# Optimization experiments

Measured on AMD Instinct MI355X. Metric: run time of the kernel, lower is better.

## Reference

```python
import jax, jax.numpy as jnp
import numpy as np

N = 50000      # nodes
E = 800000     # edges (before self-loops)
IN = 256       # in_channels
HID = 128      # hidden_channels
OUT = 128      # out_channels
NEG_SLOPE = 0.2
EPS = 1e-16


def setup_inputs() -> dict:
    key = jax.random.key(0)
    ks = jax.random.split(key, 16)
    p = lambda k, shape: jax.random.normal(k, shape, jnp.float32) * 0.1
    return {
        "x": jax.random.normal(ks[0], (N, IN), jnp.float32),
        "edge_index": jax.random.randint(ks[1], (2, E), 0, N, dtype=jnp.int64),
        # semantic MLP
        "W1": p(ks[2], (IN, HID)), "b1": jnp.zeros((HID,), jnp.float32),
        "W2": p(ks[3], (HID, HID)), "b2": jnp.zeros((HID,), jnp.float32),
        # gat1: HID -> HID//2, heads=4, concat -> 2*HID
        "g1_W": p(ks[4], (HID, 4 * (HID // 2))),
        "g1_as": p(ks[5], (4, HID // 2)), "g1_ad": p(ks[6], (4, HID // 2)),
        "g1_b": jnp.zeros((4 * (HID // 2),), jnp.float32),
        # gat2: 2*HID -> OUT, heads=2, mean -> OUT
        "g2_W": p(ks[7], (2 * HID, 2 * OUT)),
        "g2_as": p(ks[8], (2, OUT)), "g2_ad": p(ks[9], (2, OUT)),
        "g2_b": jnp.zeros((OUT,), jnp.float32),
        # gat3: OUT -> OUT, heads=1, mean -> OUT
        "g3_W": p(ks[10], (OUT, OUT)),
        "g3_as": p(ks[11], (1, OUT)), "g3_ad": p(ks[12], (1, OUT)),
        "g3_b": jnp.zeros((OUT,), jnp.float32),
    }


def _gat(h_in, src, dst, W, a_src, a_dst, bias, heads, concat, n):
    # Linear projection into heads: [n, H, C]
    h = (h_in @ W).reshape(n, heads, -1)
    alpha_s = jnp.sum(h * a_src[None], axis=-1)  # [n, H]
    alpha_d = jnp.sum(h * a_dst[None], axis=-1)  # [n, H]
    e = jax.nn.leaky_relu(alpha_s[src] + alpha_d[dst], NEG_SLOPE)  # [E', H]
    # segment softmax over edges grouped by destination node
    m = jax.ops.segment_max(e, dst, num_segments=n)
    ex = jnp.exp(e - m[dst])
    denom = jax.ops.segment_sum(ex, dst, num_segments=n)
    alpha = ex / (denom[dst] + EPS)  # [E', H]
    msg = h[src] * alpha[..., None]  # [E', H, C]
    out = jax.ops.segment_sum(msg, dst, num_segments=n)  # [n, H, C]
    out = out.reshape(n, -1) if concat else out.mean(axis=1)
    return out + bias


def reference(x, edge_index, W1, b1, W2, b2,
              g1_W, g1_as, g1_ad, g1_b,
              g2_W, g2_as, g2_ad, g2_b,
              g3_W, g3_as, g3_ad, g3_b):
    n = x.shape[0]
    # PyG GATConv add_self_loops=True: append self-loop edges once
    loops = jnp.arange(n, dtype=edge_index.dtype)
    src = jnp.concatenate([edge_index[0], loops])
    dst = jnp.concatenate([edge_index[1], loops])
    # semantic MLP (inference: dropout = identity)
    h = jax.nn.relu(x @ W1 + b1)
    h = jax.nn.relu(h @ W2 + b2)
    h = jax.nn.elu(_gat(h, src, dst, g1_W, g1_as, g1_ad, g1_b, 4, True, n))
    h = jax.nn.elu(_gat(h, src, dst, g2_W, g2_as, g2_ad, g2_b, 2, False, n))
    h = _gat(h, src, dst, g3_W, g3_as, g3_ad, g3_b, 1, False, n)
    return h
```

## Files before the change

kernel.cpp:

```cpp
#include <hip/hip_runtime.h>
#include <math.h>


#define NEG_SLOPE 0.2f
#define EPS_DEN 1e-16f

typedef __attribute__((ext_vector_type(8))) short short8;
typedef __attribute__((ext_vector_type(4))) float f32x4;
typedef __attribute__((ext_vector_type(4))) unsigned short u16x4;

__device__ inline unsigned short f2b(float f) {
  unsigned u = __builtin_bit_cast(unsigned, f);
  unsigned r = (u + 0x7fffu + ((u >> 16) & 1u)) >> 16;
  return (unsigned short)r;
}
__device__ inline float b2f(unsigned short u) {
  return __builtin_bit_cast(float, (unsigned)u << 16);
}

__device__ inline void glds16(const void* g, void* l) {
  __builtin_amdgcn_global_load_lds(
      (const __attribute__((address_space(1))) void*)g,
      (__attribute__((address_space(3))) void*)l, 16, 0, 0);
}

template <int H>
__device__ inline void loadH(const float* p, float* v) {
  if constexpr (H == 4) {
    float4 t = *(const float4*)p;
    v[0] = t.x; v[1] = t.y; v[2] = t.z; v[3] = t.w;
  } else if constexpr (H == 2) {
    float2 t = *(const float2*)p;
    v[0] = t.x; v[1] = t.y;
  } else {
    v[0] = *p;
  }
}

template <int ACT, int OBF>
__global__ __launch_bounds__(256) void mfma_gemm(
    const unsigned short* __restrict__ A, const unsigned short* __restrict__ Bt,
    const float* __restrict__ bias, float* __restrict__ Cf,
    unsigned short* __restrict__ Cb, int n, int K, int M) {
  __shared__ unsigned short As[128 * 64];
  __shared__ unsigned short Bs[128 * 64];

  const int tid = threadIdx.x;
  const int w = tid >> 6, lane = tid & 63;
  const int row0 = blockIdx.x * 128, col0 = blockIdx.y * 128;
  const int lr = lane >> 3, lg = lane & 7;
  const int lm = lane & 15, kg = lane >> 4;
  const int wm = (w >> 1) * 64, wn = (w & 1) * 64;

  f32x4 acc[4][4];
#pragma unroll
  for (int i = 0; i < 4; i++)
#pragma unroll
    for (int j = 0; j < 4; j++) acc[i][j] = {0.f, 0.f, 0.f, 0.f};

  const int swz = (lg ^ lr) << 3;

  for (int k0 = 0; k0 < K; k0 += 64) {
    __syncthreads();
#pragma unroll
    for (int it = 0; it < 4; it++) {
      const int r = w * 32 + it * 8;
      glds16(A + (size_t)(row0 + r + lr) * K + k0 + swz, &As[r * 64]);
      glds16(Bt + (size_t)(col0 + r + lr) * K + k0 + swz, &Bs[r * 64]);
    }
    __syncthreads();

#pragma unroll
    for (int kh = 0; kh < 2; kh++) {
      const int sw = ((kh * 4 + kg) ^ (lm & 7)) << 3;
      short8 aF[4], bF[4];
#pragma unroll
      for (int i = 0; i < 4; i++) {
        aF[i] = *(const short8*)&As[(wm + i * 16 + lm) * 64 + sw];
        bF[i] = *(const short8*)&Bs[(wn + i * 16 + lm) * 64 + sw];
      }
#pragma unroll
      for (int i = 0; i < 4; i++)
#pragma unroll
        for (int j = 0; j < 4; j++)
          acc[i][j] = __builtin_amdgcn_mfma_f32_16x16x32_bf16(
              aF[i], bF[j], acc[i][j], 0, 0, 0);
    }
  }

  const int r4 = kg * 4;
#pragma unroll
  for (int j = 0; j < 4; j++) {
    const int col = col0 + wn + j * 16 + lm;
    const float bv = bias ? bias[col] : 0.f;
#pragma unroll
    for (int i = 0; i < 4; i++) {
#pragma unroll
      for (int r = 0; r < 4; r++) {
        const int row = row0 + wm + i * 16 + r4 + r;
        if (row < n) {
          float v = acc[i][j][r] + bv;
          if (ACT == 1) v = v > 0.f ? v : 0.f;
          if (OBF)
            Cb[(size_t)row * M + col] = f2b(v);
          else
            Cf[(size_t)row * M + col] = v;
        }
      }
    }
  }
}

__global__ __launch_bounds__(256) void mlp_fused_kernel(
    const unsigned short* __restrict__ X, const unsigned short* __restrict__ W1t,
    const float* __restrict__ b1, const unsigned short* __restrict__ W2t,
    const float* __restrict__ b2, unsigned short* __restrict__ H2, int n) {
  __shared__ unsigned short As[128 * 64];
  __shared__ unsigned short Bs[128 * 64];
  __shared__ unsigned short H1s[128 * 136];

  const int tid = threadIdx.x;
  const int w = tid >> 6, lane = tid & 63;
  const int row0 = blockIdx.x * 128;
  const int lr = lane >> 3, lg = lane & 7;
  const int lm = lane & 15, kg = lane >> 4;
  const int wm = (w >> 1) * 64, wn = (w & 1) * 64;
  const int swz = (lg ^ lr) << 3;
  const int r4 = kg * 4;

  f32x4 acc[4][4];
#pragma unroll
  for (int i = 0; i < 4; i++)
#pragma unroll
    for (int j = 0; j < 4; j++) acc[i][j] = {0.f, 0.f, 0.f, 0.f};

  for (int k0 = 0; k0 < 256; k0 += 64) {
    __syncthreads();
#pragma unroll
    for (int it = 0; it < 4; it++) {
      const int r = w * 32 + it * 8;
      glds16(X + (size_t)(row0 + r + lr) * 256 + k0 + swz, &As[r * 64]);
      glds16(W1t + (size_t)(r + lr) * 256 + k0 + swz, &Bs[r * 64]);
    }
    __syncthreads();
#pragma unroll
    for (int kh = 0; kh < 2; kh++) {
      const int sw = ((kh * 4 + kg) ^ (lm & 7)) << 3;
      short8 aF[4], bF[4];
#pragma unroll
      for (int i = 0; i < 4; i++) {
        aF[i] = *(const short8*)&As[(wm + i * 16 + lm) * 64 + sw];
        bF[i] = *(const short8*)&Bs[(wn + i * 16 + lm) * 64 + sw];
      }
#pragma unroll
      for (int i = 0; i < 4; i++)
#pragma unroll
        for (int j = 0; j < 4; j++)
          acc[i][j] = __builtin_amdgcn_mfma_f32_16x16x32_bf16(
              aF[i], bF[j], acc[i][j], 0, 0, 0);
    }
  }

#pragma unroll
  for (int j = 0; j < 4; j++) {
    const int col = wn + j * 16 + lm;
    const float bv = b1[col];
#pragma unroll
    for (int i = 0; i < 4; i++) {
#pragma unroll
      for (int r = 0; r < 4; r++) {
        const int lrow = wm + i * 16 + r4 + r;
        float v = acc[i][j][r] + bv;
        v = v > 0.f ? v : 0.f;
        H1s[lrow * 136 + col] = f2b(v);
      }
    }
  }
#pragma unroll
  for (int i = 0; i < 4; i++)
#pragma unroll
    for (int j = 0; j < 4; j++) acc[i][j] = {0.f, 0.f, 0.f, 0.f};
  __syncthreads();

  for (int k0 = 0; k0 < 128; k0 += 64) {
    __syncthreads();
#pragma unroll
    for (int it = 0; it < 4; it++) {
      const int r = w * 32 + it * 8;
      glds16(W2t + (size_t)(r + lr) * 128 + k0 + swz, &Bs[r * 64]);
    }
    __syncthreads();
#pragma unroll
    for (int kh = 0; kh < 2; kh++) {
      const int swB = ((kh * 4 + kg) ^ (lm & 7)) << 3;
      const int kofs = k0 + (kh * 4 + kg) * 8;
      short8 aF[4], bF[4];
#pragma unroll
      for (int i = 0; i < 4; i++) {
        aF[i] = *(const short8*)&H1s[(wm + i * 16 + lm) * 136 + kofs];
        bF[i] = *(const short8*)&Bs[(wn + i * 16 + lm) * 64 + swB];
      }
#pragma unroll
      for (int i = 0; i < 4; i++)
#pragma unroll
        for (int j = 0; j < 4; j++)
          acc[i][j] = __builtin_amdgcn_mfma_f32_16x16x32_bf16(
              aF[i], bF[j], acc[i][j], 0, 0, 0);
    }
  }

#pragma unroll
  for (int j = 0; j < 4; j++) {
    const int col = wn + j * 16 + lm;
    const float bv = b2[col];
#pragma unroll
    for (int i = 0; i < 4; i++) {
#pragma unroll
      for (int r = 0; r < 4; r++) {
        const int row = row0 + wm + i * 16 + r4 + r;
        if (row < n) {
          float v = acc[i][j][r] + bv;
          v = v > 0.f ? v : 0.f;
          H2[(size_t)row * 128 + col] = f2b(v);
        }
      }
    }
  }
}

struct PrepArgs {
  const float* x; unsigned short* xb; long long nx;
  const float* W[5]; unsigned short* Wt[5];
  int K[5], M[5], t0[6];
  int* deg; int N;
};

__global__ __launch_bounds__(256) void fused_prep_kernel(PrepArgs a) {
  const int tid = threadIdx.x, bid = blockIdx.x, nb = gridDim.x;
  const long long gt = (long long)bid * 256 + tid;
  const long long gsz = (long long)nb * 256;
  __shared__ float tt[32][33];

  for (long long i = gt; i < a.N; i += gsz) a.deg[i] = 0;
  for (long long i = gt * 4; i < a.nx; i += gsz * 4) {
    float4 v = *(const float4*)(a.x + i);
    u16x4 u = {f2b(v.x), f2b(v.y), f2b(v.z), f2b(v.w)};
    *(u16x4*)(a.xb + i) = u;
  }
  for (int t = bid; t < a.t0[5]; t += nb) {
    int di = 0;
    while (t >= a.t0[di + 1]) di++;
    const int local = t - a.t0[di];
    const int K = a.K[di], M = a.M[di], mtiles = M / 32;
    const int mb = (local % mtiles) * 32, kb = (local / mtiles) * 32;
    const float* W = a.W[di];
    unsigned short* Wt = a.Wt[di];
    const int tx = tid & 31, ty = tid >> 5;
    __syncthreads();
#pragma unroll
    for (int i = 0; i < 4; i++)
      tt[ty + i * 8][tx] = W[(size_t)(kb + ty + i * 8) * M + mb + tx];
    __syncthreads();
#pragma unroll
    for (int i = 0; i < 4; i++)
      Wt[(size_t)(mb + ty + i * 8) * K + kb + tx] = f2b(tt[tx][ty + i * 8]);
  }
}

__global__ void count_deg_kernel(const int* __restrict__ edst,
                                 int* __restrict__ deg, int E, int n) {
  int i = blockIdx.x * blockDim.x + threadIdx.x;
  if (i >= E + n) return;
  int d = (i < E) ? edst[i] : (i - E);
  if ((unsigned)d < (unsigned)n) atomicAdd(&deg[d], 1);
}

__global__ __launch_bounds__(256) void block_reduce_kernel(
    const int* __restrict__ deg, int* __restrict__ bsum, int n) {
  __shared__ int s[256];
  const int t = threadIdx.x, i = blockIdx.x * 256 + t;
  s[t] = (i < n) ? deg[i] : 0;
  __syncthreads();
#pragma unroll
  for (int off = 128; off; off >>= 1) {
    if (t < off) s[t] += s[t + off];
    __syncthreads();
  }
  if (t == 0) bsum[blockIdx.x] = s[0];
}

__global__ __launch_bounds__(256) void scan_bsums_kernel(int* __restrict__ bsum,
                                                         int nb) {
  __shared__ int s[256];
  const int t = threadIdx.x;
  const int v = (t < nb) ? bsum[t] : 0;
  s[t] = v;
  __syncthreads();
#pragma unroll
  for (int off = 1; off < 256; off <<= 1) {
    int a = (t >= off) ? s[t - off] : 0;
    __syncthreads();
    s[t] += a;
    __syncthreads();
  }
  if (t < nb) bsum[t] = s[t] - v;
}

__global__ __launch_bounds__(256) void scan_final_kernel(
    const int* __restrict__ deg, const int* __restrict__ bsumx,
    int* __restrict__ rowptr, int* __restrict__ cursor, int n) {
  __shared__ int s[256];
  const int t = threadIdx.x, i = blockIdx.x * 256 + t;
  const int v = (i < n) ? deg[i] : 0;
  s[t] = v;
  __syncthreads();
#pragma unroll
  for (int off = 1; off < 256; off <<= 1) {
    int a = (t >= off) ? s[t - off] : 0;
    __syncthreads();
    s[t] += a;
    __syncthreads();
  }
  if (i < n) {
    const int base = bsumx[blockIdx.x];
    const int excl = base + s[t] - v;
    rowptr[i] = excl;
    cursor[i] = excl;
    if (i == n - 1) rowptr[n] = base + s[t];
  }
}

__global__ void scatter_kernel(const int* __restrict__ esrc,
                               const int* __restrict__ edst,
                               int* __restrict__ cursor,
                               int* __restrict__ csr_src, int E, int n) {
  int i = blockIdx.x * blockDim.x + threadIdx.x;
  int tot = E + n;
  if (i >= tot) return;
  int s, d;
  if (i < E) { s = esrc[i]; d = edst[i]; } else { s = d = i - E; }
  if ((unsigned)d >= (unsigned)n || (unsigned)s >= (unsigned)n) return;
  int pos = atomicAdd(&cursor[d], 1);
  if (pos < tot) csr_src[pos] = s;
}

template <int H, int C>
__global__ __launch_bounds__(256) void alpha_kernel(
    const unsigned short* __restrict__ proj, const float* __restrict__ a_s,
    const float* __restrict__ a_d, float* __restrict__ alpha_s,
    float* __restrict__ alpha_d, int n) {
  constexpr int HC = H * C;
  constexpr int GL = C / 4;
  const int wid = (blockIdx.x * blockDim.x + threadIdx.x) >> 6;
  const int lane = threadIdx.x & 63;
  if (wid >= n) return;
  const int c0 = lane * 4;
  float ps = 0.f, pd = 0.f;
  if (c0 < HC) {
    u16x4 raw = *(const u16x4*)(proj + (size_t)wid * HC + c0);
    float4 as = *(const float4*)(a_s + c0);
    float4 ad = *(const float4*)(a_d + c0);
    float f0 = b2f(raw.x), f1 = b2f(raw.y), f2 = b2f(raw.z), f3 = b2f(raw.w);
    ps = f0 * as.x + f1 * as.y + f2 * as.z + f3 * as.w;
    pd = f0 * ad.x + f1 * ad.y + f2 * ad.z + f3 * ad.w;
  }
#pragma unroll
  for (int off = 1; off < GL; off <<= 1) {
    ps += __shfl_xor(ps, off, 64);
    pd += __shfl_xor(pd, off, 64);
  }
  if (c0 < HC && (lane % GL) == 0) {
    int h = c0 / C;
    alpha_s[(size_t)wid * H + h] = ps;
    alpha_d[(size_t)wid * H + h] = pd;
  }
}

template <int H, int C, bool CONCAT, int ACT, int OBF>
__global__ __launch_bounds__(256) void gat_fused_kernel(
    const unsigned short* __restrict__ proj, const float* __restrict__ alpha_s,
    const float* __restrict__ alpha_d, const int* __restrict__ rowptr,
    const int* __restrict__ csr_src, const float* __restrict__ bias,
    void* __restrict__ out, int n) {
  constexpr int HC = H * C;
  constexpr int ROWSPAN = HC / 8;
  constexpr int EDGES = 64 / ROWSPAN;
  constexpr int WLANES = C / 8;

  __shared__ float exs[4][64 * H];
  __shared__ int sids[4][64];

  const int wv = threadIdx.x >> 6;
  const int wid = (blockIdx.x * blockDim.x + threadIdx.x) >> 6;
  const int lane = threadIdx.x & 63;
  if (wid >= n) return;
  const int dst = wid;
  const int eslot = lane / ROWSPAN;
  const int sl = lane % ROWSPAN;
  const int h_lane = (sl * 8) / C;
  float* myex = &exs[wv][0];
  int* mysid = &sids[wv][0];

  float adv[H];
  loadH<H>(alpha_d + (size_t)dst * H, adv);
  const int rs = rowptr[dst], re = rowptr[dst + 1];

  float denomp[H];
#pragma unroll
  for (int h = 0; h < H; h++) denomp[h] = 0.f;
  float acc[8];
#pragma unroll
  for (int k = 0; k < 8; k++) acc[k] = 0.f;

  for (int base = rs; base < re; base += 64) {
    const int cnt = min(64, re - base);
    if (lane < cnt) {
      const int s = csr_src[base + lane];
      mysid[lane] = s;
      float as[H];
      loadH<H>(alpha_s + (size_t)s * H, as);
#pragma unroll
      for (int h = 0; h < H; h++) {
        float e = as[h] + adv[h];
        e = e > 0.f ? e : NEG_SLOPE * e;
        const float ex = __expf(e);
        denomp[h] += ex;
        myex[lane * H + h] = ex;
      }
    }
    __builtin_amdgcn_wave_barrier();
    int j = eslot;
    for (; j + EDGES < cnt; j += 2 * EDGES) {
      const int s0 = mysid[j];
      const int s1 = mysid[j + EDGES];
      const float w0 = myex[j * H + h_lane];
      const float w1 = myex[(j + EDGES) * H + h_lane];
      const short8 r0 = *(const short8*)(proj + (size_t)s0 * HC + sl * 8);
      const short8 r1 = *(const short8*)(proj + (size_t)s1 * HC + sl * 8);
#pragma unroll
      for (int k = 0; k < 8; k++) acc[k] += w0 * b2f((unsigned short)r0[k]);
#pragma unroll
      for (int k = 0; k < 8; k++) acc[k] += w1 * b2f((unsigned short)r1[k]);
    }
    for (; j < cnt; j += EDGES) {
      const int s0 = mysid[j];
      const float w0 = myex[j * H + h_lane];
      const short8 r0 = *(const short8*)(proj + (size_t)s0 * HC + sl * 8);
#pragma unroll
      for (int k = 0; k < 8; k++) acc[k] += w0 * b2f((unsigned short)r0[k]);
    }
    __builtin_amdgcn_wave_barrier();
  }

#pragma unroll
  for (int off = 32; off; off >>= 1)
#pragma unroll
    for (int h = 0; h < H; h++)
      denomp[h] += __shfl_xor(denomp[h], off, 64);
#pragma unroll
  for (int off = ROWSPAN; off < 64; off <<= 1)
#pragma unroll
    for (int k = 0; k < 8; k++) acc[k] += __shfl_xor(acc[k], off, 64);

  const float inv = 1.f / (denomp[h_lane] + EPS_DEN);
  float v[8];
#pragma unroll
  for (int k = 0; k < 8; k++) v[k] = acc[k] * inv;

  if (!CONCAT && H == 2) {
#pragma unroll
    for (int k = 0; k < 8; k++) v[k] += __shfl_xor(v[k], 16, 64);
  }

  if (CONCAT) {
    if (eslot != 0) return;
    const int c0 = sl * 8;
    float vv[8];
#pragma unroll
    for (int k = 0; k < 8; k++) {
      float t = v[k] + bias[c0 + k];
      if (ACT == 1) t = t > 0.f ? t : (__expf(t) - 1.f);
      vv[k] = t;
    }
    if (OBF) {
      short8 o;
#pragma unroll
      for (int k = 0; k < 8; k++) o[k] = (short)f2b(vv[k]);
      *(short8*)((unsigned short*)out + (size_t)dst * HC + c0) = o;
    } else {
      float* op = (float*)out + (size_t)dst * HC + c0;
      *(float4*)op = make_float4(vv[0], vv[1], vv[2], vv[3]);
      *(float4*)(op + 4) = make_float4(vv[4], vv[5], vv[6], vv[7]);
    }
  } else {
    if (eslot != 0 || sl >= WLANES) return;
    const int c0 = sl * 8;
    const float invH = 1.f / (float)H;
    float vv[8];
#pragma unroll
    for (int k = 0; k < 8; k++) {
      float t = v[k] * invH + bias[c0 + k];
      if (ACT == 1) t = t > 0.f ? t : (__expf(t) - 1.f);
      vv[k] = t;
    }
    if (OBF) {
      short8 o;
#pragma unroll
      for (int k = 0; k < 8; k++) o[k] = (short)f2b(vv[k]);
      *(short8*)((unsigned short*)out + (size_t)dst * C + c0) = o;
    } else {
      float* op = (float*)out + (size_t)dst * C + c0;
      *(float4*)op = make_float4(vv[0], vv[1], vv[2], vv[3]);
      *(float4*)(op + 4) = make_float4(vv[4], vv[5], vv[6], vv[7]);
    }
  }
}

extern "C" void kernel_launch(void* const* d_in, const int* in_sizes, int n_in,
                              void* d_out, int out_size, void* d_ws,
                              size_t ws_size, hipStream_t stream) {
  const float* x    = (const float*)d_in[0];
  const int*   ei   = (const int*)d_in[1];
  const float* W1   = (const float*)d_in[2];
  const float* b1   = (const float*)d_in[3];
  const float* W2   = (const float*)d_in[4];
  const float* b2   = (const float*)d_in[5];
  const float* g1W  = (const float*)d_in[6];
  const float* g1as = (const float*)d_in[7];
  const float* g1ad = (const float*)d_in[8];
  const float* g1b  = (const float*)d_in[9];
  const float* g2W  = (const float*)d_in[10];
  const float* g2as = (const float*)d_in[11];
  const float* g2ad = (const float*)d_in[12];
  const float* g2b  = (const float*)d_in[13];
  const float* g3W  = (const float*)d_in[14];
  const float* g3as = (const float*)d_in[15];
  const float* g3ad = (const float*)d_in[16];
  const float* g3b  = (const float*)d_in[17];

  const int N = in_sizes[0] / 256;
  const int E = in_sizes[1] / 2;
  const int Etot = E + N;
  const int NT = (N + 127) / 128;
  const int NP = NT * 128;
  const int NB = (N + 255) / 256;

  char* p = (char*)d_ws;
  unsigned short* Pb  = (unsigned short*)p; p += (size_t)NP * 256 * 2;
  unsigned short* xb  = (unsigned short*)p; p += (size_t)NP * 256 * 2;
  unsigned short* h2b = (unsigned short*)p; p += (size_t)NP * 128 * 2;
  unsigned short* W1t = (unsigned short*)p; p += (size_t)128 * 256 * 2;
  unsigned short* W2t = (unsigned short*)p; p += (size_t)128 * 128 * 2;
  unsigned short* g1Wt = (unsigned short*)p; p += (size_t)256 * 128 * 2;
  unsigned short* g2Wt = (unsigned short*)p; p += (size_t)256 * 256 * 2;
  unsigned short* g3Wt = (unsigned short*)p; p += (size_t)128 * 128 * 2;
  float* alS  = (float*)p; p += (size_t)N * 4 * 4;
  float* alD  = (float*)p; p += (size_t)N * 4 * 4;
  int* deg    = (int*)p;
  int* rowptr = deg + N;
  int* cursor = rowptr + N + 1;
  int* bsum   = cursor + N;
  int* csrsrc = bsum + 256;

  const int* esrc = ei;
  const int* edst = ei + E;
  unsigned short* act1b = xb;
  unsigned short* act2b = h2b;

  PrepArgs pa;
  pa.x = x; pa.xb = xb; pa.nx = (long long)N * 256;
  pa.W[0] = W1;  pa.Wt[0] = W1t;  pa.K[0] = 256; pa.M[0] = 128;
  pa.W[1] = W2;  pa.Wt[1] = W2t;  pa.K[1] = 128; pa.M[1] = 128;
  pa.W[2] = g1W; pa.Wt[2] = g1Wt; pa.K[2] = 128; pa.M[2] = 256;
  pa.W[3] = g2W; pa.Wt[3] = g2Wt; pa.K[3] = 256; pa.M[3] = 256;
  pa.W[4] = g3W; pa.Wt[4] = g3Wt; pa.K[4] = 128; pa.M[4] = 128;
  pa.t0[0] = 0;
  for (int i = 0; i < 5; i++)
    pa.t0[i + 1] = pa.t0[i] + (pa.K[i] / 32) * (pa.M[i] / 32);
  pa.deg = deg; pa.N = N;
  fused_prep_kernel<<<512, 256, 0, stream>>>(pa);

  count_deg_kernel<<<(Etot + 255) / 256, 256, 0, stream>>>(edst, deg, E, N);
  block_reduce_kernel<<<NB, 256, 0, stream>>>(deg, bsum, N);
  scan_bsums_kernel<<<1, 256, 0, stream>>>(bsum, NB);
  scan_final_kernel<<<NB, 256, 0, stream>>>(deg, bsum, rowptr, cursor, N);
  scatter_kernel<<<(Etot + 255) / 256, 256, 0, stream>>>(esrc, edst, cursor,
                                                         csrsrc, E, N);

  mlp_fused_kernel<<<NT, 256, 0, stream>>>(xb, W1t, b1, W2t, b2, h2b, N);

  mfma_gemm<0, 1><<<dim3(NT, 2), 256, 0, stream>>>(h2b, g1Wt, nullptr, nullptr,
                                                   Pb, N, 128, 256);
  alpha_kernel<4, 64><<<(N + 3) / 4, 256, 0, stream>>>(Pb, g1as, g1ad, alS,
                                                       alD, N);
  gat_fused_kernel<4, 64, true, 1, 1><<<(N + 3) / 4, 256, 0, stream>>>(
      Pb, alS, alD, rowptr, csrsrc, g1b, act1b, N);

  mfma_gemm<0, 1><<<dim3(NT, 2), 256, 0, stream>>>(act1b, g2Wt, nullptr,
                                                   nullptr, Pb, N, 256, 256);
  alpha_kernel<2, 128><<<(N + 3) / 4, 256, 0, stream>>>(Pb, g2as, g2ad, alS,
                                                        alD, N);
  gat_fused_kernel<2, 128, false, 1, 1><<<(N + 3) / 4, 256, 0, stream>>>(
      Pb, alS, alD, rowptr, csrsrc, g2b, act2b, N);

  mfma_gemm<0, 1><<<dim3(NT, 1), 256, 0, stream>>>(act2b, g3Wt, nullptr,
                                                   nullptr, Pb, N, 128, 128);
  alpha_kernel<1, 128><<<(N + 3) / 4, 256, 0, stream>>>(Pb, g3as, g3ad, alS,
                                                        alD, N);
  gat_fused_kernel<1, 128, false, 0, 0><<<(N + 3) / 4, 256, 0, stream>>>(
      Pb, alS, alD, rowptr, csrsrc, g3b, d_out, N);
}
```

Measured before the change: 503.6 us.

## Fuse attention coefficient dots into GEMM epilogue; packed FMA gather with 4-way unroll

The separate alpha_kernel launches are removed. Each projection GEMM now computes the per-row attention dot products from its fp32 accumulators in the epilogue, using shuffles and atomicAdd into per-layer buffers that the prep kernel zeroes. The GAT aggregation loop is unrolled to four edges per iteration and uses packed v_pk_fma_f32 on bf16-unpacked pairs. This saves three launches and a re-read of the projection, and adds more loads in flight in the gather. The cost is atomics, a larger alpha buffer, and alpha values taken from fp32 accumulators rather than bf16-rounded outputs.

After: 508.9 us. Within noise of the previous version (+1.1%).

```diff
diff --git a/kernel.cpp b/kernel.cpp
--- a/kernel.cpp
+++ b/kernel.cpp
@@ -7,6 +7,7 @@
 
 typedef __attribute__((ext_vector_type(8))) short short8;
 typedef __attribute__((ext_vector_type(4))) float f32x4;
+typedef __attribute__((ext_vector_type(2))) float f32x2;
 typedef __attribute__((ext_vector_type(4))) unsigned short u16x4;
 
 __device__ inline unsigned short f2b(float f) {
@@ -22,6 +23,24 @@
   __builtin_amdgcn_global_load_lds(
       (const __attribute__((address_space(1))) void*)g,
       (__attribute__((address_space(3))) void*)l, 16, 0, 0);
+}
+
+__device__ inline f32x2 pk_fma(f32x2 a, f32x2 b, f32x2 c) {
+  f32x2 d;
+  asm("v_pk_fma_f32 %0, %1, %2, %3" : "=v"(d) : "v"(a), "v"(b), "v"(c));
+  return d;
+}
+
+__device__ inline void accum8(f32x2 acc2[4], const short8 r, float w) {
+  const f32x2 wv = {w, w};
+  const unsigned* u = (const unsigned*)&r;
+#pragma unroll
+  for (int p = 0; p < 4; p++) {
+    const unsigned lo = u[p] << 16;
+    const unsigned hi = u[p] & 0xffff0000u;
+    f32x2 val = {__builtin_bit_cast(float, lo), __builtin_bit_cast(float, hi)};
+    acc2[p] = pk_fma(val, wv, acc2[p]);
+  }
 }
 
 template <int H>
@@ -37,11 +56,13 @@
   }
 }
 
-template <int ACT, int OBF>
+template <int ACT, int OBF, int H, int CC>
 __global__ __launch_bounds__(256) void mfma_gemm(
     const unsigned short* __restrict__ A, const unsigned short* __restrict__ Bt,
     const float* __restrict__ bias, float* __restrict__ Cf,
-    unsigned short* __restrict__ Cb, int n, int K, int M) {
+    unsigned short* __restrict__ Cb, const float* __restrict__ a_s,
+    const float* __restrict__ a_d, float* __restrict__ alS,
+    float* __restrict__ alD, int n, int K, int M) {
   __shared__ unsigned short As[128 * 64];
   __shared__ unsigned short Bs[128 * 64];
 
@@ -89,6 +110,42 @@
   }
 
   const int r4 = kg * 4;
+
+  if constexpr (H > 0) {
+    const int head = (col0 + wn) / CC;
+    const int ch0 = (col0 + wn) % CC;
+    float asv[4], adv[4];
+#pragma unroll
+    for (int j = 0; j < 4; j++) {
+      asv[j] = a_s[head * CC + ch0 + j * 16 + lm];
+      adv[j] = a_d[head * CC + ch0 + j * 16 + lm];
+    }
+#pragma unroll
+    for (int i = 0; i < 4; i++) {
+#pragma unroll
+      for (int r = 0; r < 4; r++) {
+        float ps = 0.f, pd = 0.f;
+#pragma unroll
+        for (int j = 0; j < 4; j++) {
+          ps += acc[i][j][r] * asv[j];
+          pd += acc[i][j][r] * adv[j];
+        }
+#pragma unroll
+        for (int off = 1; off < 16; off <<= 1) {
+          ps += __shfl_xor(ps, off, 64);
+          pd += __shfl_xor(pd, off, 64);
+        }
+        if (lm == 0) {
+          const int row = row0 + wm + i * 16 + r4 + r;
+          if (row < n) {
+            atomicAdd(&alS[(size_t)row * H + head], ps);
+            atomicAdd(&alD[(size_t)row * H + head], pd);
+          }
+        }
+      }
+    }
+  }
+
 #pragma unroll
   for (int j = 0; j < 4; j++) {
     const int col = col0 + wn + j * 16 + lm;
@@ -233,6 +290,7 @@
   const float* W[5]; unsigned short* Wt[5];
   int K[5], M[5], t0[6];
   int* deg; int N;
+  float* alz; long long nz;
 };
 
 __global__ __launch_bounds__(256) void fused_prep_kernel(PrepArgs a) {
@@ -242,6 +300,8 @@
   __shared__ float tt[32][33];
 
   for (long long i = gt; i < a.N; i += gsz) a.deg[i] = 0;
+  for (long long i = gt * 4; i < a.nz; i += gsz * 4)
+    *(float4*)(a.alz + i) = make_float4(0.f, 0.f, 0.f, 0.f);
   for (long long i = gt * 4; i < a.nx; i += gsz * 4) {
     float4 v = *(const float4*)(a.x + i);
     u16x4 u = {f2b(v.x), f2b(v.y), f2b(v.z), f2b(v.w)};
@@ -344,38 +404,6 @@
   if (pos < tot) csr_src[pos] = s;
 }
 
-template <int H, int C>
-__global__ __launch_bounds__(256) void alpha_kernel(
-    const unsigned short* __restrict__ proj, const float* __restrict__ a_s,
-    const float* __restrict__ a_d, float* __restrict__ alpha_s,
-    float* __restrict__ alpha_d, int n) {
-  constexpr int HC = H * C;
-  constexpr int GL = C / 4;
-  const int wid = (blockIdx.x * blockDim.x + threadIdx.x) >> 6;
-  const int lane = threadIdx.x & 63;
-  if (wid >= n) return;
-  const int c0 = lane * 4;
-  float ps = 0.f, pd = 0.f;
-  if (c0 < HC) {
-    u16x4 raw = *(const u16x4*)(proj + (size_t)wid * HC + c0);
-    float4 as = *(const float4*)(a_s + c0);
-    float4 ad = *(const float4*)(a_d + c0);
-    float f0 = b2f(raw.x), f1 = b2f(raw.y), f2 = b2f(raw.z), f3 = b2f(raw.w);
-    ps = f0 * as.x + f1 * as.y + f2 * as.z + f3 * as.w;
-    pd = f0 * ad.x + f1 * ad.y + f2 * ad.z + f3 * ad.w;
-  }
-#pragma unroll
-  for (int off = 1; off < GL; off <<= 1) {
-    ps += __shfl_xor(ps, off, 64);
-    pd += __shfl_xor(pd, off, 64);
-  }
-  if (c0 < HC && (lane % GL) == 0) {
-    int h = c0 / C;
-    alpha_s[(size_t)wid * H + h] = ps;
-    alpha_d[(size_t)wid * H + h] = pd;
-  }
-}
-
 template <int H, int C, bool CONCAT, int ACT, int OBF>
 __global__ __launch_bounds__(256) void gat_fused_kernel(
     const unsigned short* __restrict__ proj, const float* __restrict__ alpha_s,
@@ -408,9 +436,11 @@
   float denomp[H];
 #pragma unroll
   for (int h = 0; h < H; h++) denomp[h] = 0.f;
-  float acc[8];
-#pragma unroll
-  for (int k = 0; k < 8; k++) acc[k] = 0.f;
+  f32x2 acc2[4];
+#pragma unroll
+  for (int p = 0; p < 4; p++) acc2[p] = {0.f, 0.f};
+
+  const unsigned short* prow = proj + sl * 8;
 
   for (int base = rs; base < re; base += 64) {
     const int cnt = min(64, re - base);
@@ -430,26 +460,38 @@
     }
     __builtin_amdgcn_wave_barrier();
     int j = eslot;
-    for (; j + EDGES < cnt; j += 2 * EDGES) {
+    for (; j + 3 * EDGES < cnt; j += 4 * EDGES) {
       const int s0 = mysid[j];
       const int s1 = mysid[j + EDGES];
+      const int s2 = mysid[j + 2 * EDGES];
+      const int s3 = mysid[j + 3 * EDGES];
       const float w0 = myex[j * H + h_lane];
       const float w1 = myex[(j + EDGES) * H + h_lane];
-      const short8 r0 = *(const short8*)(proj + (size_t)s0 * HC + sl * 8);
-      const short8 r1 = *(const short8*)(proj + (size_t)s1 * HC + sl * 8);
-#pragma unroll
-      for (int k = 0; k < 8; k++) acc[k] += w0 * b2f((unsigned short)r0[k]);
-#pragma unroll
-      for (int k = 0; k < 8; k++) acc[k] += w1 * b2f((unsigned short)r1[k]);
+      const float w2 = myex[(j + 2 * EDGES) * H + h_lane];
+      const float w3 = myex[(j + 3 * EDGES) * H + h_lane];
+      const short8 r0 = *(const short8*)(prow + (size_t)s0 * HC);
+      const short8 r1 = *(const short8*)(prow + (size_t)s1 * HC);
+      const short8 r2 = *(const short8*)(prow + (size_t)s2 * HC);
+      const short8 r3 = *(const short8*)(prow + (size_t)s3 * HC);
+      accum8(acc2, r0, w0);
+      accum8(acc2, r1, w1);
+      accum8(acc2, r2, w2);
+      accum8(acc2, r3, w3);
     }
     for (; j < cnt; j += EDGES) {
       const int s0 = mysid[j];
       const float w0 = myex[j * H + h_lane];
-      const short8 r0 = *(const short8*)(proj + (size_t)s0 * HC + sl * 8);
-#pragma unroll
-      for (int k = 0; k < 8; k++) acc[k] += w0 * b2f((unsigned short)r0[k]);
+      const short8 r0 = *(const short8*)(prow + (size_t)s0 * HC);
+      accum8(acc2, r0, w0);
     }
     __builtin_amdgcn_wave_barrier();
+  }
+
+  float acc[8];
+#pragma unroll
+  for (int p = 0; p < 4; p++) {
+    acc[2 * p] = acc2[p].x;
+    acc[2 * p + 1] = acc2[p].y;
   }
 
 #pragma unroll
@@ -554,8 +596,13 @@
   unsigned short* g1Wt = (unsigned short*)p; p += (size_t)256 * 128 * 2;
   unsigned short* g2Wt = (unsigned short*)p; p += (size_t)256 * 256 * 2;
   unsigned short* g3Wt = (unsigned short*)p; p += (size_t)128 * 128 * 2;
-  float* alS  = (float*)p; p += (size_t)N * 4 * 4;
-  float* alD  = (float*)p; p += (size_t)N * 4 * 4;
+  float* alB = (float*)p; p += (size_t)N * 14 * 4;
+  float* alS1 = alB;
+  float* alD1 = alB + (size_t)4 * N;
+  float* alS2 = alB + (size_t)8 * N;
+  float* alD2 = alB + (size_t)10 * N;
+  float* alS3 = alB + (size_t)12 * N;
+  float* alD3 = alB + (size_t)13 * N;
   int* deg    = (int*)p;
   int* rowptr = deg + N;
   int* cursor = rowptr + N + 1;
@@ -578,6 +625,7 @@
   for (int i = 0; i < 5; i++)
     pa.t0[i + 1] = pa.t0[i] + (pa.K[i] / 32) * (pa.M[i] / 32);
   pa.deg = deg; pa.N = N;
+  pa.alz = alB; pa.nz = (long long)N * 14;
   fused_prep_kernel<<<512, 256, 0, stream>>>(pa);
 
   count_deg_kernel<<<(Etot + 255) / 256, 256, 0, stream>>>(edst, deg, E, N);
@@ -589,24 +637,18 @@
 
   mlp_fused_kernel<<<NT, 256, 0, stream>>>(xb, W1t, b1, W2t, b2, h2b, N);
 
-  mfma_gemm<0, 1><<<dim3(NT, 2), 256, 0, stream>>>(h2b, g1Wt, nullptr, nullptr,
-                                                   Pb, N, 128, 256);
-  alpha_kernel<4, 64><<<(N + 3) / 4, 256, 0, stream>>>(Pb, g1as, g1ad, alS,
-                                                       alD, N);
+  mfma_gemm<0, 1, 4, 64><<<dim3(NT, 2), 256, 0, stream>>>(
+      h2b, g1Wt, nullptr, nullptr, Pb, g1as, g1ad, alS1, alD1, N, 128, 256);
   gat_fused_kernel<4, 64, true, 1, 1><<<(N + 3) / 4, 256, 0, stream>>>(
-      Pb, alS, alD, rowptr, csrsrc, g1b, act1b, N);
-
-  mfma_gemm<0, 1><<<dim3(NT, 2), 256, 0, stream>>>(act1b, g2Wt, nullptr,
-                                                   nullptr, Pb, N, 256, 256);
-  alpha_kernel<2, 128><<<(N + 3) / 4, 256, 0, stream>>>(Pb, g2as, g2ad, alS,
-                                                        alD, N);
+      Pb, alS1, alD1, rowptr, csrsrc, g1b, act1b, N);
+
+  mfma_gemm<0, 1, 2, 128><<<dim3(NT, 2), 256, 0, stream>>>(
+      act1b, g2Wt, nullptr, nullptr, Pb, g2as, g2ad, alS2, alD2, N, 256, 256);
   gat_fused_kernel<2, 128, false, 1, 1><<<(N + 3) / 4, 256, 0, stream>>>(
-      Pb, alS, alD, rowptr, csrsrc, g2b, act2b, N);
-
-  mfma_gemm<0, 1><<<dim3(NT, 1), 256, 0, stream>>>(act2b, g3Wt, nullptr,
-                                                   nullptr, Pb, N, 128, 128);
-  alpha_kernel<1, 128><<<(N + 3) / 4, 256, 0, stream>>>(Pb, g3as, g3ad, alS,
-                                                        alD, N);
+      Pb, alS2, alD2, rowptr, csrsrc, g2b, act2b, N);
+
+  mfma_gemm<0, 1, 1, 128><<<dim3(NT, 1), 256, 0, stream>>>(
+      act2b, g3Wt, nullptr, nullptr, Pb, g3as, g3ad, alS3, alD3, N, 128, 128);
   gat_fused_kernel<1, 128, false, 0, 0><<<(N + 3) / 4, 256, 0, stream>>>(
-      Pb, alS, alD, rowptr, csrsrc, g3b, d_out, N);
-}
+      Pb, alS3, alD3, rowptr, csrsrc, g3b, d_out, N);
+}
```
